# Kernel optimization log

Hardware: AMD Instinct MI355X
Metric: run time of the kernel (lower is better)

## Reference

```python
import jax, jax.numpy as jnp
import numpy as np

MARGIN = 1.0

def _pairwise_sqdist(z):
    # ||zi - zj||^2 = ||zi||^2 + ||zj||^2 - 2 zi.zj
    sq = jnp.sum(z * z, axis=-1)  # [N]
    d2 = sq[:, None] + sq[None, :] - 2.0 * (z @ z.T)
    return jnp.maximum(d2, 0.0)

def _safe_sqrt(d2):
    # sqrt with well-defined gradient at 0 (matches cdist values; diag = 0)
    pos = d2 > 0.0
    return jnp.where(pos, jnp.sqrt(jnp.where(pos, d2, 1.0)), 0.0)

def setup_inputs() -> dict:
    key = jax.random.key(0)
    k1, k2 = jax.random.split(key)
    z = jax.random.normal(k1, (8192, 128), dtype=jnp.float32)
    labels = jax.random.randint(k2, (8192,), 0, 100, dtype=jnp.int64)
    return {"z": z, "labels": labels}

def reference(z, labels):
    d2 = _pairwise_sqdist(z)              # [N, N] squared distances
    dist = _safe_sqrt(d2)                 # [N, N] distances
    label_eq = labels[:, None] == labels[None, :]
    pos = jnp.where(label_eq, d2, 0.0)
    neg = jnp.where(label_eq, 0.0, jnp.square(jax.nn.relu(MARGIN - dist)))
    return jnp.mean(pos + neg)
```

## Files before the change

### kernel.cpp

```cpp
#include <hip/hip_runtime.h>
#include <stdint.h>


#define NROWS 8192
#define DIMK  128
#define NB    64
#define NBLK  (NB * (NB + 1) / 2)

typedef __attribute__((ext_vector_type(8))) short short8;
typedef __attribute__((ext_vector_type(4))) float f32x4;

#define AS_GLOBAL __attribute__((address_space(1)))
#define AS_LDS    __attribute__((address_space(3)))

__device__ __forceinline__ unsigned short f32_to_bf16_rne(float f) {
  union { float f; uint32_t u; } v; v.f = f;
  uint32_t u = v.u;
  u += 0x7FFFu + ((u >> 16) & 1u);
  return (unsigned short)(u >> 16);
}

__global__ __launch_bounds__(256) void prep_kernel(
    const float* __restrict__ z, unsigned short* __restrict__ zb,
    float* __restrict__ sq) {
  int lane = threadIdx.x & 63, wave = threadIdx.x >> 6;
  int row = (blockIdx.x << 2) + wave;
  float2 x = ((const float2*)(z + (size_t)row * DIMK))[lane];
  unsigned short b0 = f32_to_bf16_rne(x.x);
  unsigned short b1 = f32_to_bf16_rne(x.y);
  union { uint32_t u; float f; } c0, c1;
  c0.u = (uint32_t)b0 << 16; c1.u = (uint32_t)b1 << 16;
  float s = c0.f * c0.f + c1.f * c1.f;
  ((ushort2*)(zb + (size_t)row * DIMK))[lane] = make_ushort2(b0, b1);
  #pragma unroll
  for (int off = 32; off; off >>= 1) s += __shfl_down(s, off);
  if (lane == 0) sq[row] = s;
}

__global__ __launch_bounds__(512, 4) void loss_kernel(
    const unsigned short* __restrict__ zb, const float* __restrict__ sq,
    const int* __restrict__ labels, float* __restrict__ partials) {
  __shared__ __align__(16) unsigned char ldsA[32768];
  __shared__ __align__(16) unsigned char ldsB[32768];
  __shared__ __align__(16) float sqAl[128];
  __shared__ __align__(16) float sqBl[128];
  __shared__ __align__(16) int   laAl[128];
  __shared__ __align__(16) int   laBl[128];
  __shared__ float red[8];

  int tid = threadIdx.x, lane = tid & 63, wave = tid >> 6;

  int bid = blockIdx.x;
  #define TRI(rr) ((rr) * NB - ((rr) * ((rr) - 1)) / 2)
  int r = (int)(((float)(2 * NB + 1) -
                 sqrtf((float)((2 * NB + 1) * (2 * NB + 1) - 8 * bid))) * 0.5f);
  if (r < 0) r = 0; if (r > NB - 1) r = NB - 1;
  while (TRI(r + 1) <= bid) ++r;
  while (TRI(r) > bid) --r;
  int bi = r, bj = bid - TRI(r) + r;

  const unsigned short* Ab = zb + ((size_t)bi << 7) * DIMK;
  const unsigned short* Bb = zb + ((size_t)bj << 7) * DIMK;
  #pragma unroll
  for (int t = 0; t < 4; ++t) {
    int L0 = (t << 9) + (wave << 6);
    int L  = L0 + lane;
    int rw = L >> 4;
    int c  = (L & 15) ^ (rw & 15);
    __builtin_amdgcn_global_load_lds(
        (const AS_GLOBAL void*)(uintptr_t)(Ab + rw * DIMK + (c << 3)),
        (AS_LDS void*)(uintptr_t)(ldsA + (size_t)L0 * 16), 16, 0, 0);
    __builtin_amdgcn_global_load_lds(
        (const AS_GLOBAL void*)(uintptr_t)(Bb + rw * DIMK + (c << 3)),
        (AS_LDS void*)(uintptr_t)(ldsB + (size_t)L0 * 16), 16, 0, 0);
  }
  if (tid < 128) {
    sqAl[tid] = sq[(bi << 7) + tid];
    laAl[tid] = labels[(bi << 7) + tid];
  } else if (tid < 256) {
    int t2 = tid & 127;
    sqBl[t2] = sq[(bj << 7) + t2];
    laBl[t2] = labels[(bj << 7) + t2];
  }
  asm volatile("s_waitcnt vmcnt(0)" ::: "memory");
  __syncthreads();

  int wm = wave >> 1, wn = wave & 1;
  int lc = lane & 15;
  int q  = lane >> 4;
  f32x4 acc[2][4] = {};
  #pragma unroll
  for (int ks = 0; ks < 4; ++ks) {
    int c = (ks << 2) + q;
    int p = c ^ lc;
    short8 a[2], b[4];
    #pragma unroll
    for (int i = 0; i < 2; ++i)
      a[i] = *(const short8*)(ldsA + ((wm << 5) + (i << 4) + lc) * 256 + p * 16);
    #pragma unroll
    for (int j = 0; j < 4; ++j)
      b[j] = *(const short8*)(ldsB + ((wn << 6) + (j << 4) + lc) * 256 + p * 16);
    #pragma unroll
    for (int i = 0; i < 2; ++i)
      #pragma unroll
      for (int j = 0; j < 4; ++j)
        acc[i][j] = __builtin_amdgcn_mfma_f32_16x16x32_bf16(
            a[i], b[j], acc[i][j], 0, 0, 0);
  }

  int r0 = q << 2;
  float sn_[4]; int ln_[4];
  #pragma unroll
  for (int j = 0; j < 4; ++j) {
    int n = (wn << 6) + (j << 4) + lc;
    sn_[j] = sqBl[n]; ln_[j] = laBl[n];
  }
  float ps0 = 0.f, ps1 = 0.f, ps2 = 0.f, ps3 = 0.f;
  #pragma unroll
  for (int i = 0; i < 2; ++i) {
    int mb = (wm << 5) + (i << 4) + r0;
    f32x4 sm4 = *(const f32x4*)&sqAl[mb];
    int4  lm4 = *(const int4*)&laAl[mb];
    #pragma unroll
    for (int j = 0; j < 4; ++j) {
      float d0 = fmaf(-2.f, acc[i][j][0], sm4[0] + sn_[j]);
      float d1 = fmaf(-2.f, acc[i][j][1], sm4[1] + sn_[j]);
      float d2_ = fmaf(-2.f, acc[i][j][2], sm4[2] + sn_[j]);
      float d3 = fmaf(-2.f, acc[i][j][3], sm4[3] + sn_[j]);
      float mn = fminf(fminf(d0, d1), fminf(d2_, d3));
      if (__builtin_expect(__any(mn < 1.f), 0)) {
        float dc, t;
        dc = fmaxf(d0, 0.f); t = fmaxf(1.f - sqrtf(dc), 0.f);
        ps0 += (lm4.x == ln_[j]) ? dc : t * t;
        dc = fmaxf(d1, 0.f); t = fmaxf(1.f - sqrtf(dc), 0.f);
        ps1 += (lm4.y == ln_[j]) ? dc : t * t;
        dc = fmaxf(d2_, 0.f); t = fmaxf(1.f - sqrtf(dc), 0.f);
        ps2 += (lm4.z == ln_[j]) ? dc : t * t;
        dc = fmaxf(d3, 0.f); t = fmaxf(1.f - sqrtf(dc), 0.f);
        ps3 += (lm4.w == ln_[j]) ? dc : t * t;
      } else {
        ps0 += (lm4.x == ln_[j]) ? d0 : 0.f;
        ps1 += (lm4.y == ln_[j]) ? d1 : 0.f;
        ps2 += (lm4.z == ln_[j]) ? d2_ : 0.f;
        ps3 += (lm4.w == ln_[j]) ? d3 : 0.f;
      }
    }
  }
  float psum = (ps0 + ps1) + (ps2 + ps3);
  float w = (bi == bj) ? 1.f : 2.f;
  psum *= w * (1.f / (8192.f * 8192.f));

  #pragma unroll
  for (int off = 32; off; off >>= 1) psum += __shfl_down(psum, off);
  if (lane == 0) red[wave] = psum;
  __syncthreads();
  if (tid == 0) {
    float s = 0.f;
    #pragma unroll
    for (int k = 0; k < 8; ++k) s += red[k];
    partials[bid] = s;
  }
}

__global__ __launch_bounds__(256) void reduce_kernel(
    const float* __restrict__ partials, float* __restrict__ out) {
  int tid = threadIdx.x, lane = tid & 63, wave = tid >> 6;
  float s = 0.f;
  for (int k = tid; k < NBLK; k += 256) s += partials[k];
  #pragma unroll
  for (int off = 32; off; off >>= 1) s += __shfl_down(s, off);
  __shared__ float red[4];
  if (lane == 0) red[wave] = s;
  __syncthreads();
  if (tid == 0) out[0] = red[0] + red[1] + red[2] + red[3];
}

extern "C" void kernel_launch(void* const* d_in, const int* in_sizes, int n_in,
                              void* d_out, int out_size, void* d_ws, size_t ws_size,
                              hipStream_t stream) {
  const float* z      = (const float*)d_in[0];
  const int*   labels = (const int*)d_in[1];
  float*       out    = (float*)d_out;
  unsigned short* zb  = (unsigned short*)d_ws;
  char* p = (char*)d_ws + (size_t)NROWS * DIMK * 2;
  float* sq       = (float*)p;
  float* partials = (float*)(p + NROWS * 4);

  prep_kernel<<<NROWS / 4, 256, 0, stream>>>(z, zb, sq);
  loss_kernel<<<NBLK, 512, 0, stream>>>(zb, sq, labels, partials);
  reduce_kernel<<<1, 256, 0, stream>>>(partials, out);
}
```

Before: 79.64 us.

## Switch Gram matmul from bf16 to fp8 MFMA with permuted fp8 layout

Embeddings are quantized to fp8 instead of bf16 in the prep kernel and stored with a k-permuted byte layout, so each lane can fetch all of its K-slices for the fp8 16x16x32 MFMA with two 16-byte LDS reads per tile row. The loss kernel's LDS tiles and global traffic are halved, and bf16 MFMAs are replaced by fp8 MFMAs. Squared norms are computed from the dequantized fp8 values to stay consistent. The cost is much coarser precision in the distances, which may move the loss outside tolerance.

```diff
diff --git a/kernel.cpp b/kernel.cpp
--- a/kernel.cpp
+++ b/kernel.cpp
@@ -7,41 +7,35 @@
 #define NB    64
 #define NBLK  (NB * (NB + 1) / 2)
 
-typedef __attribute__((ext_vector_type(8))) short short8;
 typedef __attribute__((ext_vector_type(4))) float f32x4;
+typedef __attribute__((ext_vector_type(2))) long long2v;
 
 #define AS_GLOBAL __attribute__((address_space(1)))
 #define AS_LDS    __attribute__((address_space(3)))
 
-__device__ __forceinline__ unsigned short f32_to_bf16_rne(float f) {
-  union { float f; uint32_t u; } v; v.f = f;
-  uint32_t u = v.u;
-  u += 0x7FFFu + ((u >> 16) & 1u);
-  return (unsigned short)(u >> 16);
-}
-
 __global__ __launch_bounds__(256) void prep_kernel(
-    const float* __restrict__ z, unsigned short* __restrict__ zb,
+    const float* __restrict__ z, unsigned char* __restrict__ zb,
     float* __restrict__ sq) {
   int lane = threadIdx.x & 63, wave = threadIdx.x >> 6;
   int row = (blockIdx.x << 2) + wave;
   float2 x = ((const float2*)(z + (size_t)row * DIMK))[lane];
-  unsigned short b0 = f32_to_bf16_rne(x.x);
-  unsigned short b1 = f32_to_bf16_rne(x.y);
-  union { uint32_t u; float f; } c0, c1;
-  c0.u = (uint32_t)b0 << 16; c1.u = (uint32_t)b1 << 16;
-  float s = c0.f * c0.f + c1.f * c1.f;
-  ((ushort2*)(zb + (size_t)row * DIMK))[lane] = make_ushort2(b0, b1);
+  int pk = __builtin_amdgcn_cvt_pk_fp8_f32(x.x, x.y, 0, false);
+  float r0 = __builtin_amdgcn_cvt_f32_fp8(pk, 0);
+  float r1 = __builtin_amdgcn_cvt_f32_fp8(pk, 1);
+  float s = r0 * r0 + r1 * r1;
+  int k = lane << 1;
+  int p = (((k >> 3) & 3) << 5) + ((k >> 5) << 3) + (k & 7);
+  *(unsigned short*)(zb + (size_t)row * DIMK + p) = (unsigned short)(pk & 0xFFFF);
   #pragma unroll
   for (int off = 32; off; off >>= 1) s += __shfl_down(s, off);
   if (lane == 0) sq[row] = s;
 }
 
 __global__ __launch_bounds__(512, 4) void loss_kernel(
-    const unsigned short* __restrict__ zb, const float* __restrict__ sq,
+    const unsigned char* __restrict__ zb, const float* __restrict__ sq,
     const int* __restrict__ labels, float* __restrict__ partials) {
-  __shared__ __align__(16) unsigned char ldsA[32768];
-  __shared__ __align__(16) unsigned char ldsB[32768];
+  __shared__ __align__(16) unsigned char ldsA[16384];
+  __shared__ __align__(16) unsigned char ldsB[16384];
   __shared__ __align__(16) float sqAl[128];
   __shared__ __align__(16) float sqBl[128];
   __shared__ __align__(16) int   laAl[128];
@@ -59,19 +53,19 @@
   while (TRI(r) > bid) --r;
   int bi = r, bj = bid - TRI(r) + r;
 
-  const unsigned short* Ab = zb + ((size_t)bi << 7) * DIMK;
-  const unsigned short* Bb = zb + ((size_t)bj << 7) * DIMK;
+  const unsigned char* Ab = zb + (((size_t)bi << 7) * DIMK);
+  const unsigned char* Bb = zb + (((size_t)bj << 7) * DIMK);
   #pragma unroll
-  for (int t = 0; t < 4; ++t) {
+  for (int t = 0; t < 2; ++t) {
     int L0 = (t << 9) + (wave << 6);
     int L  = L0 + lane;
-    int rw = L >> 4;
-    int c  = (L & 15) ^ (rw & 15);
+    int rw = L >> 3;
+    int c  = (L & 7) ^ (rw & 7);
     __builtin_amdgcn_global_load_lds(
-        (const AS_GLOBAL void*)(uintptr_t)(Ab + rw * DIMK + (c << 3)),
+        (const AS_GLOBAL void*)(uintptr_t)(Ab + rw * DIMK + (c << 4)),
         (AS_LDS void*)(uintptr_t)(ldsA + (size_t)L0 * 16), 16, 0, 0);
     __builtin_amdgcn_global_load_lds(
-        (const AS_GLOBAL void*)(uintptr_t)(Bb + rw * DIMK + (c << 3)),
+        (const AS_GLOBAL void*)(uintptr_t)(Bb + rw * DIMK + (c << 4)),
         (AS_LDS void*)(uintptr_t)(ldsB + (size_t)L0 * 16), 16, 0, 0);
   }
   if (tid < 128) {
@@ -88,25 +82,31 @@
   int wm = wave >> 1, wn = wave & 1;
   int lc = lane & 15;
   int q  = lane >> 4;
+  int x7 = lc & 7;
+  long a[2][4], b[4][4];
+  #pragma unroll
+  for (int i = 0; i < 2; ++i) {
+    const unsigned char* base = ldsA + ((wm << 5) + (i << 4) + lc) * 128;
+    long2v lo = *(const long2v*)(base + ((((q << 1)    ) ^ x7) << 4));
+    long2v hi = *(const long2v*)(base + ((((q << 1) + 1) ^ x7) << 4));
+    a[i][0] = lo.x; a[i][1] = lo.y; a[i][2] = hi.x; a[i][3] = hi.y;
+  }
+  #pragma unroll
+  for (int j = 0; j < 4; ++j) {
+    const unsigned char* base = ldsB + ((wn << 6) + (j << 4) + lc) * 128;
+    long2v lo = *(const long2v*)(base + ((((q << 1)    ) ^ x7) << 4));
+    long2v hi = *(const long2v*)(base + ((((q << 1) + 1) ^ x7) << 4));
+    b[j][0] = lo.x; b[j][1] = lo.y; b[j][2] = hi.x; b[j][3] = hi.y;
+  }
   f32x4 acc[2][4] = {};
   #pragma unroll
-  for (int ks = 0; ks < 4; ++ks) {
-    int c = (ks << 2) + q;
-    int p = c ^ lc;
-    short8 a[2], b[4];
-    #pragma unroll
-    for (int i = 0; i < 2; ++i)
-      a[i] = *(const short8*)(ldsA + ((wm << 5) + (i << 4) + lc) * 256 + p * 16);
-    #pragma unroll
-    for (int j = 0; j < 4; ++j)
-      b[j] = *(const short8*)(ldsB + ((wn << 6) + (j << 4) + lc) * 256 + p * 16);
+  for (int ks = 0; ks < 4; ++ks)
     #pragma unroll
     for (int i = 0; i < 2; ++i)
       #pragma unroll
       for (int j = 0; j < 4; ++j)
-        acc[i][j] = __builtin_amdgcn_mfma_f32_16x16x32_bf16(
-            a[i], b[j], acc[i][j], 0, 0, 0);
-  }
+        acc[i][j] = __builtin_amdgcn_mfma_f32_16x16x32_fp8_fp8(
+            a[i][ks], b[j][ks], acc[i][j], 0, 0, 0);
 
   int r0 = q << 2;
   float sn_[4]; int ln_[4];
@@ -123,26 +123,26 @@
     int4  lm4 = *(const int4*)&laAl[mb];
     #pragma unroll
     for (int j = 0; j < 4; ++j) {
-      float d0 = fmaf(-2.f, acc[i][j][0], sm4[0] + sn_[j]);
-      float d1 = fmaf(-2.f, acc[i][j][1], sm4[1] + sn_[j]);
+      float d0  = fmaf(-2.f, acc[i][j][0], sm4[0] + sn_[j]);
+      float d1  = fmaf(-2.f, acc[i][j][1], sm4[1] + sn_[j]);
       float d2_ = fmaf(-2.f, acc[i][j][2], sm4[2] + sn_[j]);
-      float d3 = fmaf(-2.f, acc[i][j][3], sm4[3] + sn_[j]);
+      float d3  = fmaf(-2.f, acc[i][j][3], sm4[3] + sn_[j]);
       float mn = fminf(fminf(d0, d1), fminf(d2_, d3));
       if (__builtin_expect(__any(mn < 1.f), 0)) {
         float dc, t;
-        dc = fmaxf(d0, 0.f); t = fmaxf(1.f - sqrtf(dc), 0.f);
+        dc = fmaxf(d0, 0.f);  t = fmaxf(1.f - sqrtf(dc), 0.f);
         ps0 += (lm4.x == ln_[j]) ? dc : t * t;
-        dc = fmaxf(d1, 0.f); t = fmaxf(1.f - sqrtf(dc), 0.f);
+        dc = fmaxf(d1, 0.f);  t = fmaxf(1.f - sqrtf(dc), 0.f);
         ps1 += (lm4.y == ln_[j]) ? dc : t * t;
         dc = fmaxf(d2_, 0.f); t = fmaxf(1.f - sqrtf(dc), 0.f);
         ps2 += (lm4.z == ln_[j]) ? dc : t * t;
-        dc = fmaxf(d3, 0.f); t = fmaxf(1.f - sqrtf(dc), 0.f);
+        dc = fmaxf(d3, 0.f);  t = fmaxf(1.f - sqrtf(dc), 0.f);
         ps3 += (lm4.w == ln_[j]) ? dc : t * t;
       } else {
-        ps0 += (lm4.x == ln_[j]) ? d0 : 0.f;
-        ps1 += (lm4.y == ln_[j]) ? d1 : 0.f;
+        ps0 += (lm4.x == ln_[j]) ? d0  : 0.f;
+        ps1 += (lm4.y == ln_[j]) ? d1  : 0.f;
         ps2 += (lm4.z == ln_[j]) ? d2_ : 0.f;
-        ps3 += (lm4.w == ln_[j]) ? d3 : 0.f;
+        ps3 += (lm4.w == ln_[j]) ? d3  : 0.f;
       }
     }
   }
@@ -181,8 +181,8 @@
   const float* z      = (const float*)d_in[0];
   const int*   labels = (const int*)d_in[1];
   float*       out    = (float*)d_out;
-  unsigned short* zb  = (unsigned short*)d_ws;
-  char* p = (char*)d_ws + (size_t)NROWS * DIMK * 2;
+  unsigned char* zb   = (unsigned char*)d_ws;
+  char* p = (char*)d_ws + (size_t)NROWS * DIMK;
   float* sq       = (float*)p;
   float* partials = (float*)(p + NROWS * 4);
 
```

Result: faster. 76.27 us (-4.2%).
